# Kernel optimization log

Measured on AMD Instinct MI355X. Metric: run time of the kernel, lower is better.

## Reference

```python
import jax, jax.numpy as jnp
import numpy as np

D, K = 128, 32
B, H, W = 32, 96, 96


def setup_inputs() -> dict:
    key = jax.random.key(0)
    k1, k2, k3 = jax.random.split(key, 3)
    X = jax.random.normal(k1, (B, D, H, W), dtype=jnp.float32)
    std1 = 1.0 / float(np.sqrt(K * D))
    codewords = jax.random.uniform(k2, (K, D), dtype=jnp.float32, minval=-std1, maxval=std1)
    scale = jax.random.uniform(k3, (K,), dtype=jnp.float32, minval=-1.0, maxval=0.0)
    return {"X": X, "codewords": codewords, "scale": scale}


def reference(X, codewords, scale):
    b, d = X.shape[0], X.shape[1]
    # [B, D, H, W] -> [B, N, D]
    Xf = X.reshape(b, d, -1).transpose(0, 2, 1)
    # scale_l2: SL[b,n,k] = scale_k^2 * ||x_bn - c_k||^2 (no (B,N,K,D) materialization)
    x2 = jnp.sum(Xf * Xf, axis=-1)                      # [B, N]
    c2 = jnp.sum(codewords * codewords, axis=-1)        # [K]
    xc = jnp.einsum('bnd,kd->bnk', Xf, codewords)       # [B, N, K]
    sl = (scale * scale)[None, None, :] * (x2[:, :, None] - 2.0 * xc + c2[None, None, :])
    A = jax.nn.softmax(sl, axis=2)                      # [B, N, K]
    # aggregate: E[b,k,d] = sum_n A[b,n,k] * (x[b,n,d] - c[k,d])
    E = jnp.einsum('bnk,bnd->bkd', A, Xf) - jnp.sum(A, axis=1)[:, :, None] * codewords[None, :, :]
    return E
```

## Files before the change

kernel.cpp:

```cpp
#include <hip/hip_runtime.h>

#define B_ 32
#define D_ 128
#define K_ 32
#define N_ 9216
#define NT 256
#define NS 64
#define XDN_S 72
#define AKN_S 72
#define X2S_S 68

typedef __bf16 bf16x8_t __attribute__((ext_vector_type(8)));
typedef float f32x4_t __attribute__((ext_vector_type(4)));

__device__ __forceinline__ unsigned short f2bf(float f) {
    unsigned u = __float_as_uint(f);
    u = (u + 0x7fffu + ((u >> 16) & 1u)) >> 16;
    return (unsigned short)u;
}
__device__ __forceinline__ unsigned f2bf_pk(float lo, float hi) {
    unsigned a = __float_as_uint(lo);
    a = (a + 0x7fffu + ((a >> 16) & 1u)) >> 16;
    unsigned b = __float_as_uint(hi);
    b = (b + 0x7fffu + ((b >> 16) & 1u)) & 0xffff0000u;
    return a | b;
}

__global__ __launch_bounds__(256, 3) void k_fused(
        const float* __restrict__ X, const float* __restrict__ cw,
        const float* __restrict__ scale, float* __restrict__ ws) {
    __shared__ __align__(16) unsigned short X_nd[NS * 128];
    __shared__ __align__(16) unsigned short X_dn[D_ * XDN_S];
    __shared__ __align__(16) unsigned short CWb[K_ * 128];
    __shared__ __align__(16) unsigned short Akn[K_ * AKN_S];
    __shared__ float x2s[16 * X2S_S];
    __shared__ float x2f[NS];
    __shared__ float u_s[K_], w_s[K_];
    __shared__ float sAw[4 * 34];
    __shared__ float sA[K_];

    const int t = threadIdx.x;
    const int w = t >> 6;
    const int l = t & 63;
    const int lm = l & 15;
    const int lq = l >> 4;
    const int b = blockIdx.x / 36;
    const int n0 = (blockIdx.x % 36) * NT;

    #pragma unroll
    for (int i = 0; i < 4; ++i) {
        int idx = t + 256 * i;
        int k = idx >> 5, d4 = idx & 31;
        float4 c = ((const float4*)cw)[idx];
        int phys = (d4 >> 1) ^ (k & 15);
        unsigned* p = (unsigned*)&CWb[k * 128 + phys * 8 + (d4 & 1) * 4];
        p[0] = f2bf_pk(c.x, c.y);
        p[1] = f2bf_pk(c.z, c.w);
    }
    if (t < 32) {
        float sc = scale[t];
        float s2 = sc * sc;
        const float4* cr = (const float4*)(cw + t * 128);
        float c2 = 0.f;
        #pragma unroll 8
        for (int i = 0; i < 32; ++i) {
            float4 v = cr[i];
            c2 += v.x * v.x + v.y * v.y + v.z * v.z + v.w * v.w;
        }
        u_s[t] = s2;
        w_s[t] = s2 * c2;
    }
    __syncthreads();
    const float u0 = u_s[lm], u1 = u_s[16 + lm];
    const float w0 = w_s[lm], w1 = w_s[16 + lm];

    f32x4_t acc2[2][2];
    #pragma unroll
    for (int a = 0; a < 2; ++a)
        #pragma unroll
        for (int c = 0; c < 2; ++c)
            acc2[a][c] = (f32x4_t){0.f, 0.f, 0.f, 0.f};
    float ps0 = 0.f, ps1 = 0.f;

    const int n4 = t & 15;
    const int d8 = t >> 4;

    for (int s = 0; s < 4; ++s) {
        __syncthreads();
        const float* Xg = X + ((size_t)b * D_ + d8 * 8) * N_ + n0 + s * NS + n4 * 4;
        float4 v[8];
        #pragma unroll
        for (int j = 0; j < 8; ++j) v[j] = *(const float4*)(Xg + (size_t)j * N_);
        #pragma unroll
        for (int jn = 0; jn < 4; ++jn) {
            float a = 0.f;
            #pragma unroll
            for (int j = 0; j < 8; ++j) {
                float xv = (&v[j].x)[jn];
                a += xv * xv;
            }
            x2s[d8 * X2S_S + n4 * 4 + jn] = a;
        }
        #pragma unroll
        for (int j = 0; j < 8; ++j) {
            unsigned* p = (unsigned*)&X_dn[(d8 * 8 + j) * XDN_S + n4 * 4];
            p[0] = f2bf_pk(v[j].x, v[j].y);
            p[1] = f2bf_pk(v[j].z, v[j].w);
        }
        #pragma unroll
        for (int jn = 0; jn < 4; ++jn) {
            unsigned q[4];
            #pragma unroll
            for (int j2 = 0; j2 < 4; ++j2)
                q[j2] = f2bf_pk((&v[2 * j2].x)[jn], (&v[2 * j2 + 1].x)[jn]);
            int row = n4 * 4 + jn;
            *(uint4*)&X_nd[row * 128 + (d8 ^ (row & 15)) * 8] = *(const uint4*)q;
        }
        __syncthreads();
        if (t < NS) {
            float a = 0.f;
            #pragma unroll
            for (int g = 0; g < 16; ++g) a += x2s[g * X2S_S + t];
            x2f[t] = a;
        }
        f32x4_t acc1[2];
        acc1[0] = (f32x4_t){0.f, 0.f, 0.f, 0.f};
        acc1[1] = (f32x4_t){0.f, 0.f, 0.f, 0.f};
        #pragma unroll
        for (int ks = 0; ks < 4; ++ks) {
            int g = (ks * 4 + lq) ^ lm;
            bf16x8_t a  = *(const bf16x8_t*)&X_nd[(w * 16 + lm) * 128 + g * 8];
            bf16x8_t b0 = *(const bf16x8_t*)&CWb[lm * 128 + g * 8];
            bf16x8_t b1 = *(const bf16x8_t*)&CWb[(16 + lm) * 128 + g * 8];
            acc1[0] = __builtin_amdgcn_mfma_f32_16x16x32_bf16(a, b0, acc1[0], 0, 0, 0);
            acc1[1] = __builtin_amdgcn_mfma_f32_16x16x32_bf16(a, b1, acc1[1], 0, 0, 0);
        }
        __syncthreads();
        #pragma unroll
        for (int r = 0; r < 4; ++r) {
            int nl = w * 16 + lq * 4 + r;
            float x2v = x2f[nl];
            float sl0 = u0 * x2v + w0 - 2.f * u0 * acc1[0][r];
            float sl1 = u1 * x2v + w1 - 2.f * u1 * acc1[1][r];
            float m = fmaxf(sl0, sl1);
            m = fmaxf(m, __shfl_xor(m, 1));
            m = fmaxf(m, __shfl_xor(m, 2));
            m = fmaxf(m, __shfl_xor(m, 4));
            m = fmaxf(m, __shfl_xor(m, 8));
            float p0 = __expf(sl0 - m);
            float p1 = __expf(sl1 - m);
            float sum = p0 + p1;
            sum += __shfl_xor(sum, 1);
            sum += __shfl_xor(sum, 2);
            sum += __shfl_xor(sum, 4);
            sum += __shfl_xor(sum, 8);
            float inv = 1.f / sum;
            p0 *= inv; p1 *= inv;
            ps0 += p0; ps1 += p1;
            Akn[lm * AKN_S + nl] = f2bf(p0);
            Akn[(16 + lm) * AKN_S + nl] = f2bf(p1);
        }
        __syncthreads();
        #pragma unroll
        for (int ks = 0; ks < 2; ++ks) {
            bf16x8_t xa0 = *(const bf16x8_t*)&X_dn[(w * 16 + lm) * XDN_S + ks * 32 + lq * 8];
            bf16x8_t xa1 = *(const bf16x8_t*)&X_dn[((w + 4) * 16 + lm) * XDN_S + ks * 32 + lq * 8];
            bf16x8_t pb0 = *(const bf16x8_t*)&Akn[lm * AKN_S + ks * 32 + lq * 8];
            bf16x8_t pb1 = *(const bf16x8_t*)&Akn[(16 + lm) * AKN_S + ks * 32 + lq * 8];
            acc2[0][0] = __builtin_amdgcn_mfma_f32_16x16x32_bf16(xa0, pb0, acc2[0][0], 0, 0, 0);
            acc2[0][1] = __builtin_amdgcn_mfma_f32_16x16x32_bf16(xa0, pb1, acc2[0][1], 0, 0, 0);
            acc2[1][0] = __builtin_amdgcn_mfma_f32_16x16x32_bf16(xa1, pb0, acc2[1][0], 0, 0, 0);
            acc2[1][1] = __builtin_amdgcn_mfma_f32_16x16x32_bf16(xa1, pb1, acc2[1][1], 0, 0, 0);
        }
    }

    ps0 += __shfl_xor(ps0, 16); ps0 += __shfl_xor(ps0, 32);
    ps1 += __shfl_xor(ps1, 16); ps1 += __shfl_xor(ps1, 32);
    if (l < 16) {
        sAw[w * 34 + l] = ps0;
        sAw[w * 34 + 16 + l] = ps1;
    }
    __syncthreads();
    if (t < 32) sA[t] = sAw[t] + sAw[34 + t] + sAw[68 + t] + sAw[102 + t];
    __syncthreads();

    float* pout = ws + (size_t)blockIdx.x * (K_ * D_);
    #pragma unroll
    for (int di = 0; di < 2; ++di) {
        #pragma unroll
        for (int kt = 0; kt < 2; ++kt) {
            #pragma unroll
            for (int r = 0; r < 4; ++r) {
                int d = (w + di * 4) * 16 + lq * 4 + r;
                int k = kt * 16 + lm;
                pout[k * 128 + d] = acc2[di][kt][r] - sA[k] * cw[k * 128 + d];
            }
        }
    }
}

__global__ __launch_bounds__(256) void k_reduce(
        const float* __restrict__ ws, float* __restrict__ out) {
    int i = blockIdx.x * 256 + threadIdx.x;
    int b = i >> 10;
    int j = i & 1023;
    const float4* p = (const float4*)ws + (size_t)b * 36 * 1024 + j;
    float4 s = make_float4(0.f, 0.f, 0.f, 0.f);
    #pragma unroll
    for (int c = 0; c < 36; ++c) {
        float4 v = p[(size_t)c * 1024];
        s.x += v.x; s.y += v.y; s.z += v.z; s.w += v.w;
    }
    ((float4*)out)[i] = s;
}

extern "C" void kernel_launch(void* const* d_in, const int* in_sizes, int n_in,
                              void* d_out, int out_size, void* d_ws, size_t ws_size,
                              hipStream_t stream) {
    const float* X     = (const float*)d_in[0];
    const float* cw    = (const float*)d_in[1];
    const float* scale = (const float*)d_in[2];
    float* out = (float*)d_out;
    float* ws  = (float*)d_ws;

    k_fused <<<dim3(B_ * 36), dim3(256), 0, stream>>>(X, cw, scale, ws);
    k_reduce<<<dim3(128),     dim3(256), 0, stream>>>(ws, out);
}
```

Measured before the change: 227.9 us.

## Make each wave own its 16-row X slice to drop block barriers

Remaps the global X load so each wave loads all 128 d values for its own 16 n-rows. The x2 row norms are then reduced with wave shuffles instead of a shared-memory scratch array plus a second pass. The first MFMA stage then reads only wave-local X_nd rows, so two block-wide __syncthreads are replaced by an LDS waitcnt and a wave barrier. X_dn stores are rotated by dgrp to spread LDS bank use, and a barrier is added before the final sAw write. Global loads are now less contiguous per wave, and correctness depends on the wave-local data ownership holding.

Measured after the change: 316.4 us. 38.9% more time.

```diff
diff --git a/kernel.cpp b/kernel.cpp
--- a/kernel.cpp
+++ b/kernel.cpp
@@ -8,7 +8,6 @@
 #define NS 64
 #define XDN_S 72
 #define AKN_S 72
-#define X2S_S 68
 
 typedef __bf16 bf16x8_t __attribute__((ext_vector_type(8)));
 typedef float f32x4_t __attribute__((ext_vector_type(4)));
@@ -33,8 +32,6 @@
     __shared__ __align__(16) unsigned short X_dn[D_ * XDN_S];
     __shared__ __align__(16) unsigned short CWb[K_ * 128];
     __shared__ __align__(16) unsigned short Akn[K_ * AKN_S];
-    __shared__ float x2s[16 * X2S_S];
-    __shared__ float x2f[NS];
     __shared__ float u_s[K_], w_s[K_];
     __shared__ float sAw[4 * 34];
     __shared__ float sA[K_];
@@ -44,6 +41,8 @@
     const int l = t & 63;
     const int lm = l & 15;
     const int lq = l >> 4;
+    const int nq = l & 3;
+    const int dgrp = l >> 2;
     const int b = blockIdx.x / 36;
     const int n0 = (blockIdx.x % 36) * NT;
 
@@ -82,15 +81,14 @@
             acc2[a][c] = (f32x4_t){0.f, 0.f, 0.f, 0.f};
     float ps0 = 0.f, ps1 = 0.f;
 
-    const int n4 = t & 15;
-    const int d8 = t >> 4;
-
     for (int s = 0; s < 4; ++s) {
         __syncthreads();
-        const float* Xg = X + ((size_t)b * D_ + d8 * 8) * N_ + n0 + s * NS + n4 * 4;
+        const float* Xg = X + (size_t)b * (D_ * (size_t)N_) + n0 + s * NS + w * 16 + nq * 4;
         float4 v[8];
         #pragma unroll
-        for (int j = 0; j < 8; ++j) v[j] = *(const float4*)(Xg + (size_t)j * N_);
+        for (int j = 0; j < 8; ++j)
+            v[j] = *(const float4*)(Xg + (size_t)(dgrp * 8 + j) * N_);
+        float x2p[4];
         #pragma unroll
         for (int jn = 0; jn < 4; ++jn) {
             float a = 0.f;
@@ -99,13 +97,21 @@
                 float xv = (&v[j].x)[jn];
                 a += xv * xv;
             }
-            x2s[d8 * X2S_S + n4 * 4 + jn] = a;
+            x2p[jn] = a;
+        }
+        #pragma unroll
+        for (int jn = 0; jn < 4; ++jn) {
+            x2p[jn] += __shfl_xor(x2p[jn], 4);
+            x2p[jn] += __shfl_xor(x2p[jn], 8);
+            x2p[jn] += __shfl_xor(x2p[jn], 16);
+            x2p[jn] += __shfl_xor(x2p[jn], 32);
         }
         #pragma unroll
         for (int j = 0; j < 8; ++j) {
-            unsigned* p = (unsigned*)&X_dn[(d8 * 8 + j) * XDN_S + n4 * 4];
-            p[0] = f2bf_pk(v[j].x, v[j].y);
-            p[1] = f2bf_pk(v[j].z, v[j].w);
+            int jj = (j + dgrp) & 7;
+            unsigned* p = (unsigned*)&X_dn[(dgrp * 8 + jj) * XDN_S + w * 16 + nq * 4];
+            p[0] = f2bf_pk(v[jj].x, v[jj].y);
+            p[1] = f2bf_pk(v[jj].z, v[jj].w);
         }
         #pragma unroll
         for (int jn = 0; jn < 4; ++jn) {
@@ -113,16 +119,11 @@
             #pragma unroll
             for (int j2 = 0; j2 < 4; ++j2)
                 q[j2] = f2bf_pk((&v[2 * j2].x)[jn], (&v[2 * j2 + 1].x)[jn]);
-            int row = n4 * 4 + jn;
-            *(uint4*)&X_nd[row * 128 + (d8 ^ (row & 15)) * 8] = *(const uint4*)q;
-        }
-        __syncthreads();
-        if (t < NS) {
-            float a = 0.f;
-            #pragma unroll
-            for (int g = 0; g < 16; ++g) a += x2s[g * X2S_S + t];
-            x2f[t] = a;
-        }
+            int row = w * 16 + nq * 4 + jn;
+            *(uint4*)&X_nd[row * 128 + ((dgrp ^ (row & 15)) * 8)] = *(const uint4*)q;
+        }
+        asm volatile("s_waitcnt lgkmcnt(0)" ::: "memory");
+        __builtin_amdgcn_wave_barrier();
         f32x4_t acc1[2];
         acc1[0] = (f32x4_t){0.f, 0.f, 0.f, 0.f};
         acc1[1] = (f32x4_t){0.f, 0.f, 0.f, 0.f};
@@ -135,11 +136,10 @@
             acc1[0] = __builtin_amdgcn_mfma_f32_16x16x32_bf16(a, b0, acc1[0], 0, 0, 0);
             acc1[1] = __builtin_amdgcn_mfma_f32_16x16x32_bf16(a, b1, acc1[1], 0, 0, 0);
         }
-        __syncthreads();
         #pragma unroll
         for (int r = 0; r < 4; ++r) {
             int nl = w * 16 + lq * 4 + r;
-            float x2v = x2f[nl];
+            float x2v = __shfl(x2p[r], lq);
             float sl0 = u0 * x2v + w0 - 2.f * u0 * acc1[0][r];
             float sl1 = u1 * x2v + w1 - 2.f * u1 * acc1[1][r];
             float m = fmaxf(sl0, sl1);
@@ -176,6 +176,7 @@
 
     ps0 += __shfl_xor(ps0, 16); ps0 += __shfl_xor(ps0, 32);
     ps1 += __shfl_xor(ps1, 16); ps1 += __shfl_xor(ps1, 32);
+    __syncthreads();
     if (l < 16) {
         sAw[w * 34 + l] = ps0;
         sAw[w * 34 + 16 + l] = ps1;
```

## Prefetch next X chunk into registers and trim block barriers in fused kernel

Applied to the files above, without the earlier changes.

Global loads for the next 64-column X chunk are issued at the top of each iteration and kept in registers. This lets the HBM fetch overlap the current chunk's bf16 conversion, MFMA and softmax work. Plain __syncthreads is replaced by an inline-asm barrier that waits only on LDS counters, so the outstanding global loads are not drained at each barrier. The x2 row-norm reduction is now done redundantly per lane and broadcast with shuffles, which removes one barrier and the x2f buffer. Output stores are vectorised to float4. The trade-off is higher register pressure from the extra 32 prefetch registers, plus some leftover redundant shuffle statements.

Measured after the change: 226.9 us. No clear change (-0.4%).

```diff
diff --git a/kernel.cpp b/kernel.cpp
--- a/kernel.cpp
+++ b/kernel.cpp
@@ -25,6 +25,9 @@
     b = (b + 0x7fffu + ((b >> 16) & 1u)) & 0xffff0000u;
     return a | b;
 }
+__device__ __forceinline__ void bar_lds() {
+    asm volatile("s_waitcnt lgkmcnt(0)\n\ts_barrier" ::: "memory");
+}
 
 __global__ __launch_bounds__(256, 3) void k_fused(
         const float* __restrict__ X, const float* __restrict__ cw,
@@ -34,7 +37,6 @@
     __shared__ __align__(16) unsigned short CWb[K_ * 128];
     __shared__ __align__(16) unsigned short Akn[K_ * AKN_S];
     __shared__ float x2s[16 * X2S_S];
-    __shared__ float x2f[NS];
     __shared__ float u_s[K_], w_s[K_];
     __shared__ float sAw[4 * 34];
     __shared__ float sA[K_];
@@ -44,6 +46,8 @@
     const int l = t & 63;
     const int lm = l & 15;
     const int lq = l >> 4;
+    const int d8 = t >> 4;
+    const int n4 = t & 15;
     const int b = blockIdx.x / 36;
     const int n0 = (blockIdx.x % 36) * NT;
 
@@ -82,15 +86,19 @@
             acc2[a][c] = (f32x4_t){0.f, 0.f, 0.f, 0.f};
     float ps0 = 0.f, ps1 = 0.f;
 
-    const int n4 = t & 15;
-    const int d8 = t >> 4;
+    const float* Xg = X + ((size_t)b * D_ + d8 * 8) * N_ + n0 + n4 * 4;
+    float4 v[8];
+    #pragma unroll
+    for (int j = 0; j < 8; ++j) v[j] = *(const float4*)(Xg + (size_t)j * N_);
 
     for (int s = 0; s < 4; ++s) {
-        __syncthreads();
-        const float* Xg = X + ((size_t)b * D_ + d8 * 8) * N_ + n0 + s * NS + n4 * 4;
-        float4 v[8];
-        #pragma unroll
-        for (int j = 0; j < 8; ++j) v[j] = *(const float4*)(Xg + (size_t)j * N_);
+        bar_lds();
+        float4 vn[8];
+        if (s < 3) {
+            const float* Xg2 = Xg + (s + 1) * NS;
+            #pragma unroll
+            for (int j = 0; j < 8; ++j) vn[j] = *(const float4*)(Xg2 + (size_t)j * N_);
+        }
         #pragma unroll
         for (int jn = 0; jn < 4; ++jn) {
             float a = 0.f;
@@ -114,15 +122,12 @@
             for (int j2 = 0; j2 < 4; ++j2)
                 q[j2] = f2bf_pk((&v[2 * j2].x)[jn], (&v[2 * j2 + 1].x)[jn]);
             int row = n4 * 4 + jn;
-            *(uint4*)&X_nd[row * 128 + (d8 ^ (row & 15)) * 8] = *(const uint4*)q;
-        }
-        __syncthreads();
-        if (t < NS) {
-            float a = 0.f;
-            #pragma unroll
-            for (int g = 0; g < 16; ++g) a += x2s[g * X2S_S + t];
-            x2f[t] = a;
-        }
+            *(uint4*)&X_nd[row * 128 + ((d8 ^ (row & 15)) * 8)] = *(const uint4*)q;
+        }
+        bar_lds();
+        float x2row = 0.f;
+        #pragma unroll
+        for (int g = 0; g < 16; ++g) x2row += x2s[g * X2S_S + l];
         f32x4_t acc1[2];
         acc1[0] = (f32x4_t){0.f, 0.f, 0.f, 0.f};
         acc1[1] = (f32x4_t){0.f, 0.f, 0.f, 0.f};
@@ -135,11 +140,12 @@
             acc1[0] = __builtin_amdgcn_mfma_f32_16x16x32_bf16(a, b0, acc1[0], 0, 0, 0);
             acc1[1] = __builtin_amdgcn_mfma_f32_16x16x32_bf16(a, b1, acc1[1], 0, 0, 0);
         }
-        __syncthreads();
         #pragma unroll
         for (int r = 0; r < 4; ++r) {
             int nl = w * 16 + lq * 4 + r;
-            float x2v = x2f[nl];
+            float x2v = __shfl(x2row, lq * 4 + r + w * 16 - w * 16);
+            x2v = __shfl(x2row, lq * 4 + r);
+            x2v = __shfl(x2row, nl);
             float sl0 = u0 * x2v + w0 - 2.f * u0 * acc1[0][r];
             float sl1 = u1 * x2v + w1 - 2.f * u1 * acc1[1][r];
             float m = fmaxf(sl0, sl1);
@@ -160,7 +166,7 @@
             Akn[lm * AKN_S + nl] = f2bf(p0);
             Akn[(16 + lm) * AKN_S + nl] = f2bf(p1);
         }
-        __syncthreads();
+        bar_lds();
         #pragma unroll
         for (int ks = 0; ks < 2; ++ks) {
             bf16x8_t xa0 = *(const bf16x8_t*)&X_dn[(w * 16 + lm) * XDN_S + ks * 32 + lq * 8];
@@ -172,10 +178,15 @@
             acc2[1][0] = __builtin_amdgcn_mfma_f32_16x16x32_bf16(xa1, pb0, acc2[1][0], 0, 0, 0);
             acc2[1][1] = __builtin_amdgcn_mfma_f32_16x16x32_bf16(xa1, pb1, acc2[1][1], 0, 0, 0);
         }
+        if (s < 3) {
+            #pragma unroll
+            for (int j = 0; j < 8; ++j) v[j] = vn[j];
+        }
     }
 
     ps0 += __shfl_xor(ps0, 16); ps0 += __shfl_xor(ps0, 32);
     ps1 += __shfl_xor(ps1, 16); ps1 += __shfl_xor(ps1, 32);
+    __syncthreads();
     if (l < 16) {
         sAw[w * 34 + l] = ps0;
         sAw[w * 34 + 16 + l] = ps1;
@@ -189,12 +200,13 @@
     for (int di = 0; di < 2; ++di) {
         #pragma unroll
         for (int kt = 0; kt < 2; ++kt) {
-            #pragma unroll
-            for (int r = 0; r < 4; ++r) {
-                int d = (w + di * 4) * 16 + lq * 4 + r;
-                int k = kt * 16 + lm;
-                pout[k * 128 + d] = acc2[di][kt][r] - sA[k] * cw[k * 128 + d];
-            }
+            const int d0 = (w + di * 4) * 16 + lq * 4;
+            const int k  = kt * 16 + lm;
+            float4 o;
+            #pragma unroll
+            for (int r = 0; r < 4; ++r)
+                (&o.x)[r] = acc2[di][kt][r] - sA[k] * cw[k * 128 + d0 + r];
+            *(float4*)&pout[k * 128 + d0] = o;
         }
     }
 }
```
